# Kernel optimization log

Measured on AMD Instinct MI355X. Metric: run time of the kernel, lower is better.

The kernel has to match this reference:

```python
import jax, jax.numpy as jnp
import numpy as np

B, S, D = 4, 4096, 64

def setup_inputs() -> dict:
    key = jax.random.key(0)
    kq, kk, kv = jax.random.split(key, 3)
    return {
        "q": jax.random.normal(kq, (B, S, D), dtype=jnp.float32),
        "k": jax.random.normal(kk, (B, S, D), dtype=jnp.float32),
        "v": jax.random.normal(kv, (B, S, D), dtype=jnp.float32),
    }

def reference(q, k, v):
    # scores: [B, Sq, Sk]; NOTE: scale is k.shape[-1] (not sqrt), per the source.
    scores = jnp.einsum("bqd,bkd->bqk", q, k) / k.shape[-1]
    # softmax over dim=1 == the QUERY axis (non-standard), then matmul V.
    probs = jax.nn.softmax(scores, axis=1)            # [B, Sq, Sk]
    attn = jnp.einsum("bqk,bkd->bqd", probs, v)       # [B, Sq, D]
    attn_w = jax.nn.softmax(attn, axis=1)             # softmax over Sq again
    return (attn, attn_w)
```

## Files before the change

### kernel.cpp

```cpp
#include <hip/hip_runtime.h>
#include <hip/hip_bf16.h>
#include <math.h>

#define BB 4
#define SS 4096
#define DD 64
#define KSPLIT 4
#define QSPLIT 8

typedef __attribute__((ext_vector_type(8))) short short8;
typedef __attribute__((ext_vector_type(4))) float f32x4;
typedef __attribute__((ext_vector_type(2))) unsigned int u32x2;
typedef unsigned int u32;
typedef unsigned short ushort_t;

#define MFMA16(a,b,c) __builtin_amdgcn_mfma_f32_16x16x32_bf16((a),(b),(c),0,0,0)
#define C2SC 0.022542110700140054f

union Pk8 { short8 s8; u32 u[4]; u32x2 h[2]; };

static __device__ __forceinline__ unsigned short f2bf(float f) {
  union { float f; u32 u; } x; x.f = f;
  u32 r = (x.u + 0x7FFFu + ((x.u >> 16) & 1u)) >> 16;
  return (unsigned short)r;
}

static __device__ __forceinline__ u32 pk2(float a, float b) {
  return (u32)f2bf(a) | ((u32)f2bf(b) << 16);
}

static __device__ __forceinline__ void gload16(const void* g, void* l) {
  __builtin_amdgcn_global_load_lds((const __attribute__((address_space(1))) u32*)g,
                                   (__attribute__((address_space(3))) u32*)l, 16, 0, 0);
}

__global__ __launch_bounds__(256) void p0_convert(
    const float* __restrict__ q, const float* __restrict__ k,
    ushort_t* __restrict__ QB, ushort_t* __restrict__ KB,
    float* __restrict__ out0, float* __restrict__ z2)
{
  const size_t i = (size_t)blockIdx.x * 256 + threadIdx.x;
  float4 a = ((const float4*)q)[i];
  float4 c = ((const float4*)k)[i];
  ((ushort4*)QB)[i] = make_ushort4(f2bf(a.x), f2bf(a.y), f2bf(a.z), f2bf(a.w));
  ((ushort4*)KB)[i] = make_ushort4(f2bf(c.x), f2bf(c.y), f2bf(c.z), f2bf(c.w));
  ((float4*)out0)[i] = make_float4(0.f, 0.f, 0.f, 0.f);
  if (blockIdx.x == 0) z2[threadIdx.x] = 0.f;
}

__global__ __launch_bounds__(256, 4) void pa_colsum(
    const ushort_t* __restrict__ QB, const ushort_t* __restrict__ KB,
    float* __restrict__ Zp)
{
  const int kb0 = blockIdx.x * 128;
  const int qch = blockIdx.y;
  const int b   = blockIdx.z;
  const int t = threadIdx.x, w = t >> 6, lane = t & 63;
  const int g = lane >> 4, r15 = lane & 15;
  const int r8 = lane >> 3, c8 = lane & 7;
  const int QCH = SS / QSPLIT;
  const int NT = QCH / 64;

  __shared__ alignas(16) char qbuf[2][64*128];

  short8 ak[2][2];
#pragma unroll
  for (int s = 0; s < 2; ++s)
#pragma unroll
    for (int dh = 0; dh < 2; ++dh)
      ak[s][dh] = *(const short8*)(KB + ((size_t)b*SS + kb0 + 32*w + 16*s + r15)*DD + 32*dh + 8*g);

  {
    const int q0 = qch * QCH;
#pragma unroll
    for (int j = 0; j < 2; ++j) {
      const int rl = 16*w + 8*j + r8;
      const char* gsrc = (const char*)(QB + ((size_t)b*SS + q0 + rl)*DD) + 16*(c8 ^ r8);
      gload16(gsrc, qbuf[0] + (16*w + 8*j)*128);
    }
  }
  asm volatile("s_waitcnt vmcnt(0)" ::: "memory");
  __syncthreads();

  float z[8];
#pragma unroll
  for (int i = 0; i < 8; ++i) z[i] = 0.f;

  int cur = 0;
  for (int tt = 0; tt < NT; ++tt) {
    if (tt < NT-1) {
      const int q0 = qch*QCH + (tt+1)*64;
#pragma unroll
      for (int j = 0; j < 2; ++j) {
        const int rl = 16*w + 8*j + r8;
        const char* gsrc = (const char*)(QB + ((size_t)b*SS + q0 + rl)*DD) + 16*(c8 ^ r8);
        gload16(gsrc, qbuf[cur^1] + (16*w + 8*j)*128);
      }
    }
    const char* qb = qbuf[cur];
#pragma unroll
    for (int qt = 0; qt < 4; ++qt) {
      const int qrow = 16*qt + r15;
      const char* base = qb + qrow*128;
      short8 bq0 = *(const short8*)(base + 16*((g    ) ^ (qrow & 7)));
      short8 bq1 = *(const short8*)(base + 16*((4 + g) ^ (qrow & 7)));
#pragma unroll
      for (int s = 0; s < 2; ++s) {
        f32x4 acc = {0.f,0.f,0.f,0.f};
        acc = MFMA16(ak[s][0], bq0, acc);
        acc = MFMA16(ak[s][1], bq1, acc);
        z[4*s+0] += exp2f(acc[0]*C2SC); z[4*s+1] += exp2f(acc[1]*C2SC);
        z[4*s+2] += exp2f(acc[2]*C2SC); z[4*s+3] += exp2f(acc[3]*C2SC);
      }
    }
    asm volatile("s_waitcnt vmcnt(0)" ::: "memory");
    __syncthreads();
    cur ^= 1;
  }
#pragma unroll
  for (int m = 1; m < 16; m <<= 1)
#pragma unroll
    for (int i = 0; i < 8; ++i) z[i] += __shfl_xor(z[i], m);
  if (r15 == 0) {
#pragma unroll
    for (int s = 0; s < 2; ++s)
#pragma unroll
      for (int r = 0; r < 4; ++r)
        Zp[((size_t)qch*BB + b)*SS + kb0 + 32*w + 16*s + 4*g + r] = z[4*s+r];
  }
}

__global__ __launch_bounds__(256) void p2_vt(
    const float* __restrict__ v, const float* __restrict__ Zp,
    ushort_t* __restrict__ VT)
{
  const int k0 = blockIdx.x * 64;
  const int b  = blockIdx.y;
  const int t = threadIdx.x;
  __shared__ float vs[64][65];
  __shared__ float izs[64];
  {
    const int row = t >> 2, cq = (t & 3) * 16;
    const float* src = v + ((size_t)b*SS + k0 + row)*DD + cq;
#pragma unroll
    for (int i = 0; i < 4; ++i) {
      float4 x = ((const float4*)src)[i];
      vs[row][cq + 4*i + 0] = x.x; vs[row][cq + 4*i + 1] = x.y;
      vs[row][cq + 4*i + 2] = x.z; vs[row][cq + 4*i + 3] = x.w;
    }
  }
  if (t < 64) {
    float z = 0.f;
#pragma unroll
    for (int c = 0; c < QSPLIT; ++c)
      z += Zp[((size_t)c*BB + b)*SS + k0 + t];
    izs[t] = 1.0f / z;
  }
  __syncthreads();
  const int d = t >> 2, ks = (t & 3) * 16;
  u32* dst = (u32*)VT + (((size_t)b*DD + d)*SS + k0 + ks)/2;
#pragma unroll
  for (int i = 0; i < 8; ++i) {
    float a0 = vs[ks + 2*i    ][d] * izs[ks + 2*i    ];
    float a1 = vs[ks + 2*i + 1][d] * izs[ks + 2*i + 1];
    dst[i] = (u32)f2bf(a0) | ((u32)f2bf(a1) << 16);
  }
}

__global__ __launch_bounds__(256, 3) void pb_attn(
    const ushort_t* __restrict__ QB, const ushort_t* __restrict__ KB,
    const ushort_t* __restrict__ VT, float* __restrict__ out0)
{
  const int q0 = blockIdx.x * 64;
  const int kbase = blockIdx.y * (SS / KSPLIT);
  const int b  = blockIdx.z;
  const int t = threadIdx.x, w = t >> 6, lane = t & 63;
  const int g = lane >> 4, r15 = lane & 15;
  const int NT = SS / KSPLIT / 128;

  __shared__ alignas(16) char kbuf[128*128];
  __shared__ alignas(16) char vbuf[64*256];

  short8 aq[4][2];
#pragma unroll
  for (int qt = 0; qt < 4; ++qt)
#pragma unroll
    for (int dh = 0; dh < 2; ++dh)
      aq[qt][dh] = *(const short8*)(QB + ((size_t)b*SS + q0 + 16*qt + r15)*DD + 32*dh + 8*g);

  f32x4 acc[4][4];
#pragma unroll
  for (int qt = 0; qt < 4; ++qt)
#pragma unroll
    for (int dt = 0; dt < 4; ++dt) acc[qt][dt] = (f32x4){0.f,0.f,0.f,0.f};

  for (int kt = 0; kt < NT; ++kt) {
    const int k0 = kbase + kt*128;
#pragma unroll
    for (int j = 0; j < 4; ++j) {
      const int row = 32*j + 8*w + (lane >> 3);
      const char* gsrc = (const char*)(KB + ((size_t)b*SS + k0 + row)*DD) + 16*((lane & 7) ^ (row & 7));
      gload16(gsrc, kbuf + (32*j + 8*w)*128);
    }
#pragma unroll
    for (int j = 0; j < 4; ++j) {
      const int row = 16*j + 4*w + (lane >> 4);
      const char* gsrc = (const char*)(VT + ((size_t)b*DD + row)*SS + k0) + 16*((lane & 15) ^ (row & 15));
      gload16(gsrc, vbuf + (16*j + 4*w)*256);
    }
    asm volatile("s_waitcnt vmcnt(0)" ::: "memory");
    __syncthreads();

    u32 pk[2][4][2];
#pragma unroll
    for (int s = 0; s < 2; ++s) {
      const int rowA = 64*s + 16*w + r15;
      const char* base = kbuf + rowA*128;
      short8 ka0 = *(const short8*)(base + 16*((g    ) ^ (rowA & 7)));
      short8 ka1 = *(const short8*)(base + 16*((4 + g) ^ (rowA & 7)));
#pragma unroll
      for (int qt = 0; qt < 4; ++qt) {
        f32x4 a = {0.f,0.f,0.f,0.f};
        a = MFMA16(ka0, aq[qt][0], a);
        a = MFMA16(ka1, aq[qt][1], a);
        pk[s][qt][0] = pk2(exp2f(a[0]*C2SC), exp2f(a[1]*C2SC));
        pk[s][qt][1] = pk2(exp2f(a[2]*C2SC), exp2f(a[3]*C2SC));
      }
    }
    Pk8 ap[4];
#pragma unroll
    for (int qt = 0; qt < 4; ++qt) {
      ap[qt].u[0] = pk[0][qt][0]; ap[qt].u[1] = pk[0][qt][1];
      ap[qt].u[2] = pk[1][qt][0]; ap[qt].u[3] = pk[1][qt][1];
    }
    const int cA = 2*w + (g >> 1);
    const int cB = 8 + 2*w + (g >> 1);
    const int sub8 = 8*(g & 1);
#pragma unroll
    for (int dt = 0; dt < 4; ++dt) {
      const int vrow = 16*dt + r15;
      Pk8 bv;
      bv.h[0] = *(const u32x2*)(vbuf + vrow*256 + 16*(cA ^ r15) + sub8);
      bv.h[1] = *(const u32x2*)(vbuf + vrow*256 + 16*(cB ^ r15) + sub8);
#pragma unroll
      for (int qt = 0; qt < 4; ++qt)
        acc[qt][dt] = MFMA16(ap[qt].s8, bv.s8, acc[qt][dt]);
    }
    __syncthreads();
  }

  f32x4* r0 = (f32x4*)kbuf;
  f32x4* r1 = (f32x4*)vbuf;
  if (w == 1) {
#pragma unroll
    for (int qt = 0; qt < 4; ++qt)
#pragma unroll
      for (int dt = 0; dt < 4; ++dt) r0[(qt*4+dt)*64 + lane] = acc[qt][dt];
  }
  if (w == 2) {
#pragma unroll
    for (int qt = 0; qt < 4; ++qt)
#pragma unroll
      for (int dt = 0; dt < 4; ++dt) r1[(qt*4+dt)*64 + lane] = acc[qt][dt];
  }
  __syncthreads();
  if (w == 0) {
#pragma unroll
    for (int qt = 0; qt < 4; ++qt)
#pragma unroll
      for (int dt = 0; dt < 4; ++dt)
        acc[qt][dt] += r0[(qt*4+dt)*64 + lane] + r1[(qt*4+dt)*64 + lane];
  }
  __syncthreads();
  if (w == 3) {
#pragma unroll
    for (int qt = 0; qt < 4; ++qt)
#pragma unroll
      for (int dt = 0; dt < 4; ++dt) r0[(qt*4+dt)*64 + lane] = acc[qt][dt];
  }
  __syncthreads();
  if (w == 0) {
#pragma unroll
    for (int qt = 0; qt < 4; ++qt)
#pragma unroll
      for (int dt = 0; dt < 4; ++dt) {
        f32x4 s = acc[qt][dt] + r0[(qt*4+dt)*64 + lane];
#pragma unroll
        for (int rr = 0; rr < 4; ++rr)
          atomicAdd(&out0[((size_t)b*SS + q0 + 16*qt + 4*g + rr)*DD + 16*dt + r15], s[rr]);
      }
  }
}

__global__ __launch_bounds__(256) void k4f(
    const float* __restrict__ attn, float* __restrict__ z2)
{
  const int b = blockIdx.x;
  const int q0 = blockIdx.y * 32;
  const int t = threadIdx.x;
  const int d = t & 63, rg = t >> 6;
  float ze = 0.f;
#pragma unroll
  for (int i = 0; i < 8; ++i) {
    float a = attn[((size_t)b*SS + q0 + 4*i + rg)*DD + d];
    ze += __expf(a);
  }
  __shared__ float red[4][64];
  red[rg][d] = ze;
  __syncthreads();
  if (t < 64)
    atomicAdd(&z2[b*DD + t], red[0][t] + red[1][t] + red[2][t] + red[3][t]);
}

__global__ __launch_bounds__(256) void k6w(
    const float* __restrict__ attn, const float* __restrict__ z2,
    float* __restrict__ out1)
{
  const size_t i = (size_t)blockIdx.x * 256 + threadIdx.x;
  const int b = (int)(i >> 18);
  const int d = (int)(i & 63);
  out1[i] = __expf(attn[i]) / z2[b*DD + d];
}

extern "C" void kernel_launch(void* const* d_in, const int* in_sizes, int n_in,
                              void* d_out, int out_size, void* d_ws, size_t ws_size,
                              hipStream_t stream) {
  const float* q = (const float*)d_in[0];
  const float* k = (const float*)d_in[1];
  const float* v = (const float*)d_in[2];
  float* out0 = (float*)d_out;
  float* out1 = out0 + (size_t)BB * SS * DD;

  ushort_t* QB = (ushort_t*)out1;
  ushort_t* KB = QB + (size_t)BB * SS * DD;

  float* ws = (float*)d_ws;
  ushort_t* VT = (ushort_t*)ws;
  float* Zp = (float*)(VT + (size_t)BB * DD * SS);
  float* z2 = Zp + (size_t)QSPLIT * BB * SS;

  hipLaunchKernelGGL(p0_convert, dim3(BB*SS*DD/4/256), dim3(256), 0, stream, q, k, QB, KB, out0, z2);
  hipLaunchKernelGGL(pa_colsum, dim3(SS/128, QSPLIT, BB), dim3(256), 0, stream, QB, KB, Zp);
  hipLaunchKernelGGL(p2_vt, dim3(SS/64, BB), dim3(256), 0, stream, v, Zp, VT);
  hipLaunchKernelGGL(pb_attn, dim3(SS/64, KSPLIT, BB), dim3(256), 0, stream, QB, KB, VT, out0);
  hipLaunchKernelGGL(k4f, dim3(BB, SS/32), dim3(256), 0, stream, out0, z2);
  hipLaunchKernelGGL(k6w, dim3(BB*SS*DD/256), dim3(256), 0, stream, out0, z2, out1);
}
```

Measured before the change: 87.79 us.

## Replace LDS staging with direct register double-buffered global loads in colsum and attn

Both the column-sum and attention kernels stop staging Q/K/V tiles through shared memory with global_load_lds and barriers. Each wave now loads its MFMA operands straight from global memory into registers, alternating between two register buffers so the next tile's loads overlap the current tile's compute. The attention kernel's final cross-wave reduction now uses a single shared array and one barrier, and its occupancy hint drops to 2 blocks per SM to make room for the extra registers. pk2 switches to the library bf16 conversion. The trade-off is more redundant global/L2 traffic and register pressure in exchange for removing LDS round-trips and per-tile barriers.

```diff
diff --git a/kernel.cpp b/kernel.cpp
--- a/kernel.cpp
+++ b/kernel.cpp
@@ -26,12 +26,11 @@
 }
 
 static __device__ __forceinline__ u32 pk2(float a, float b) {
-  return (u32)f2bf(a) | ((u32)f2bf(b) << 16);
-}
-
-static __device__ __forceinline__ void gload16(const void* g, void* l) {
-  __builtin_amdgcn_global_load_lds((const __attribute__((address_space(1))) u32*)g,
-                                   (__attribute__((address_space(3))) u32*)l, 16, 0, 0);
+  __hip_bfloat16 lo = __float2bfloat16(a);
+  __hip_bfloat16 hi = __float2bfloat16(b);
+  unsigned short ls, hs;
+  __builtin_memcpy(&ls, &lo, 2); __builtin_memcpy(&hs, &hi, 2);
+  return (u32)ls | ((u32)hs << 16);
 }
 
 __global__ __launch_bounds__(256) void p0_convert(
@@ -48,6 +47,31 @@
   if (blockIdx.x == 0) z2[threadIdx.x] = 0.f;
 }
 
+static __device__ __forceinline__ void load_q4(
+    short8 bq[4][2], const ushort_t* __restrict__ QB, size_t qrow, int g)
+{
+#pragma unroll
+  for (int qt = 0; qt < 4; ++qt)
+#pragma unroll
+    for (int dh = 0; dh < 2; ++dh)
+      bq[qt][dh] = *(const short8*)(QB + (qrow + 16*qt)*DD + 32*dh + 8*g);
+}
+
+static __device__ __forceinline__ void pa_tile(
+    const short8 ak[2][2], const short8 bq[4][2], float z[8])
+{
+#pragma unroll
+  for (int qt = 0; qt < 4; ++qt)
+#pragma unroll
+    for (int s = 0; s < 2; ++s) {
+      f32x4 a = {0.f,0.f,0.f,0.f};
+      a = MFMA16(ak[s][0], bq[qt][0], a);
+      a = MFMA16(ak[s][1], bq[qt][1], a);
+      z[4*s+0] += exp2f(a[0]*C2SC); z[4*s+1] += exp2f(a[1]*C2SC);
+      z[4*s+2] += exp2f(a[2]*C2SC); z[4*s+3] += exp2f(a[3]*C2SC);
+    }
+}
+
 __global__ __launch_bounds__(256, 4) void pa_colsum(
     const ushort_t* __restrict__ QB, const ushort_t* __restrict__ KB,
     float* __restrict__ Zp)
@@ -57,11 +81,7 @@
   const int b   = blockIdx.z;
   const int t = threadIdx.x, w = t >> 6, lane = t & 63;
   const int g = lane >> 4, r15 = lane & 15;
-  const int r8 = lane >> 3, c8 = lane & 7;
   const int QCH = SS / QSPLIT;
-  const int NT = QCH / 64;
-
-  __shared__ alignas(16) char qbuf[2][64*128];
 
   short8 ak[2][2];
 #pragma unroll
@@ -70,53 +90,22 @@
     for (int dh = 0; dh < 2; ++dh)
       ak[s][dh] = *(const short8*)(KB + ((size_t)b*SS + kb0 + 32*w + 16*s + r15)*DD + 32*dh + 8*g);
 
-  {
-    const int q0 = qch * QCH;
-#pragma unroll
-    for (int j = 0; j < 2; ++j) {
-      const int rl = 16*w + 8*j + r8;
-      const char* gsrc = (const char*)(QB + ((size_t)b*SS + q0 + rl)*DD) + 16*(c8 ^ r8);
-      gload16(gsrc, qbuf[0] + (16*w + 8*j)*128);
-    }
-  }
-  asm volatile("s_waitcnt vmcnt(0)" ::: "memory");
-  __syncthreads();
-
   float z[8];
 #pragma unroll
   for (int i = 0; i < 8; ++i) z[i] = 0.f;
 
-  int cur = 0;
-  for (int tt = 0; tt < NT; ++tt) {
-    if (tt < NT-1) {
-      const int q0 = qch*QCH + (tt+1)*64;
-#pragma unroll
-      for (int j = 0; j < 2; ++j) {
-        const int rl = 16*w + 8*j + r8;
-        const char* gsrc = (const char*)(QB + ((size_t)b*SS + q0 + rl)*DD) + 16*(c8 ^ r8);
-        gload16(gsrc, qbuf[cur^1] + (16*w + 8*j)*128);
-      }
-    }
-    const char* qb = qbuf[cur];
-#pragma unroll
-    for (int qt = 0; qt < 4; ++qt) {
-      const int qrow = 16*qt + r15;
-      const char* base = qb + qrow*128;
-      short8 bq0 = *(const short8*)(base + 16*((g    ) ^ (qrow & 7)));
-      short8 bq1 = *(const short8*)(base + 16*((4 + g) ^ (qrow & 7)));
-#pragma unroll
-      for (int s = 0; s < 2; ++s) {
-        f32x4 acc = {0.f,0.f,0.f,0.f};
-        acc = MFMA16(ak[s][0], bq0, acc);
-        acc = MFMA16(ak[s][1], bq1, acc);
-        z[4*s+0] += exp2f(acc[0]*C2SC); z[4*s+1] += exp2f(acc[1]*C2SC);
-        z[4*s+2] += exp2f(acc[2]*C2SC); z[4*s+3] += exp2f(acc[3]*C2SC);
-      }
-    }
-    asm volatile("s_waitcnt vmcnt(0)" ::: "memory");
-    __syncthreads();
-    cur ^= 1;
-  }
+  const size_t qrow0 = (size_t)b*SS + qch*QCH + r15;
+  short8 bqA[4][2], bqB[4][2];
+  load_q4(bqA, QB, qrow0, g);
+
+#pragma unroll 1
+  for (int tt = 0; tt < QCH/64; tt += 2) {
+    load_q4(bqB, QB, qrow0 + (size_t)(tt+1)*64, g);
+    pa_tile(ak, bqA, z);
+    if (tt + 2 < QCH/64) load_q4(bqA, QB, qrow0 + (size_t)(tt+2)*64, g);
+    pa_tile(ak, bqB, z);
+  }
+
 #pragma unroll
   for (int m = 1; m < 16; m <<= 1)
 #pragma unroll
@@ -167,7 +156,55 @@
   }
 }
 
-__global__ __launch_bounds__(256, 3) void pb_attn(
+static __device__ __forceinline__ void load_k2(
+    short8 ka[2][2], const ushort_t* __restrict__ KB, size_t krow, int g)
+{
+#pragma unroll
+  for (int s = 0; s < 2; ++s)
+#pragma unroll
+    for (int dh = 0; dh < 2; ++dh)
+      ka[s][dh] = *(const short8*)(KB + (krow + 64*s)*DD + 32*dh + 8*g);
+}
+
+static __device__ __forceinline__ void load_v4(
+    short8 bv[4], const ushort_t* __restrict__ VT, size_t voff)
+{
+#pragma unroll
+  for (int dt = 0; dt < 4; ++dt) {
+    Pk8 u;
+    u.h[0] = *(const u32x2*)(VT + voff + (size_t)16*dt*SS);
+    u.h[1] = *(const u32x2*)(VT + voff + (size_t)16*dt*SS + 64);
+    bv[dt] = u.s8;
+  }
+}
+
+static __device__ __forceinline__ void pb_tile(
+    const short8 ka[2][2], const short8 bv[4], const short8 aq[4][2],
+    f32x4 acc[4][4])
+{
+  u32 pk[2][4][2];
+#pragma unroll
+  for (int s = 0; s < 2; ++s)
+#pragma unroll
+    for (int qt = 0; qt < 4; ++qt) {
+      f32x4 a = {0.f,0.f,0.f,0.f};
+      a = MFMA16(ka[s][0], aq[qt][0], a);
+      a = MFMA16(ka[s][1], aq[qt][1], a);
+      pk[s][qt][0] = pk2(exp2f(a[0]*C2SC), exp2f(a[1]*C2SC));
+      pk[s][qt][1] = pk2(exp2f(a[2]*C2SC), exp2f(a[3]*C2SC));
+    }
+#pragma unroll
+  for (int qt = 0; qt < 4; ++qt) {
+    Pk8 ap;
+    ap.u[0] = pk[0][qt][0]; ap.u[1] = pk[0][qt][1];
+    ap.u[2] = pk[1][qt][0]; ap.u[3] = pk[1][qt][1];
+#pragma unroll
+    for (int dt = 0; dt < 4; ++dt)
+      acc[qt][dt] = MFMA16(ap.s8, bv[dt], acc[qt][dt]);
+  }
+}
+
+__global__ __launch_bounds__(256, 2) void pb_attn(
     const ushort_t* __restrict__ QB, const ushort_t* __restrict__ KB,
     const ushort_t* __restrict__ VT, float* __restrict__ out0)
 {
@@ -178,8 +215,7 @@
   const int g = lane >> 4, r15 = lane & 15;
   const int NT = SS / KSPLIT / 128;
 
-  __shared__ alignas(16) char kbuf[128*128];
-  __shared__ alignas(16) char vbuf[64*256];
+  __shared__ f32x4 red[3][16][64];
 
   short8 aq[4][2];
 #pragma unroll
@@ -194,97 +230,39 @@
 #pragma unroll
     for (int dt = 0; dt < 4; ++dt) acc[qt][dt] = (f32x4){0.f,0.f,0.f,0.f};
 
-  for (int kt = 0; kt < NT; ++kt) {
-    const int k0 = kbase + kt*128;
-#pragma unroll
-    for (int j = 0; j < 4; ++j) {
-      const int row = 32*j + 8*w + (lane >> 3);
-      const char* gsrc = (const char*)(KB + ((size_t)b*SS + k0 + row)*DD) + 16*((lane & 7) ^ (row & 7));
-      gload16(gsrc, kbuf + (32*j + 8*w)*128);
+  const size_t krow0 = (size_t)b*SS + kbase + 16*w + r15;
+  const size_t voff0 = ((size_t)b*DD + r15)*SS + kbase + 16*w + 4*g;
+
+  short8 kaA[2][2], kaB[2][2], bvA[4], bvB[4];
+  load_k2(kaA, KB, krow0, g);
+  load_v4(bvA, VT, voff0);
+
+#pragma unroll 1
+  for (int kt = 0; kt < NT; kt += 2) {
+    load_k2(kaB, KB, krow0 + (size_t)(kt+1)*128, g);
+    load_v4(bvB, VT, voff0 + (size_t)(kt+1)*128);
+    pb_tile(kaA, bvA, aq, acc);
+    if (kt + 2 < NT) {
+      load_k2(kaA, KB, krow0 + (size_t)(kt+2)*128, g);
+      load_v4(bvA, VT, voff0 + (size_t)(kt+2)*128);
     }
-#pragma unroll
-    for (int j = 0; j < 4; ++j) {
-      const int row = 16*j + 4*w + (lane >> 4);
-      const char* gsrc = (const char*)(VT + ((size_t)b*DD + row)*SS + k0) + 16*((lane & 15) ^ (row & 15));
-      gload16(gsrc, vbuf + (16*j + 4*w)*256);
-    }
-    asm volatile("s_waitcnt vmcnt(0)" ::: "memory");
-    __syncthreads();
-
-    u32 pk[2][4][2];
-#pragma unroll
-    for (int s = 0; s < 2; ++s) {
-      const int rowA = 64*s + 16*w + r15;
-      const char* base = kbuf + rowA*128;
-      short8 ka0 = *(const short8*)(base + 16*((g    ) ^ (rowA & 7)));
-      short8 ka1 = *(const short8*)(base + 16*((4 + g) ^ (rowA & 7)));
-#pragma unroll
-      for (int qt = 0; qt < 4; ++qt) {
-        f32x4 a = {0.f,0.f,0.f,0.f};
-        a = MFMA16(ka0, aq[qt][0], a);
-        a = MFMA16(ka1, aq[qt][1], a);
-        pk[s][qt][0] = pk2(exp2f(a[0]*C2SC), exp2f(a[1]*C2SC));
-        pk[s][qt][1] = pk2(exp2f(a[2]*C2SC), exp2f(a[3]*C2SC));
-      }
-    }
-    Pk8 ap[4];
-#pragma unroll
-    for (int qt = 0; qt < 4; ++qt) {
-      ap[qt].u[0] = pk[0][qt][0]; ap[qt].u[1] = pk[0][qt][1];
-      ap[qt].u[2] = pk[1][qt][0]; ap[qt].u[3] = pk[1][qt][1];
-    }
-    const int cA = 2*w + (g >> 1);
-    const int cB = 8 + 2*w + (g >> 1);
-    const int sub8 = 8*(g & 1);
-#pragma unroll
-    for (int dt = 0; dt < 4; ++dt) {
-      const int vrow = 16*dt + r15;
-      Pk8 bv;
-      bv.h[0] = *(const u32x2*)(vbuf + vrow*256 + 16*(cA ^ r15) + sub8);
-      bv.h[1] = *(const u32x2*)(vbuf + vrow*256 + 16*(cB ^ r15) + sub8);
-#pragma unroll
-      for (int qt = 0; qt < 4; ++qt)
-        acc[qt][dt] = MFMA16(ap[qt].s8, bv.s8, acc[qt][dt]);
-    }
-    __syncthreads();
-  }
-
-  f32x4* r0 = (f32x4*)kbuf;
-  f32x4* r1 = (f32x4*)vbuf;
-  if (w == 1) {
+    pb_tile(kaB, bvB, aq, acc);
+  }
+
+  if (w > 0) {
 #pragma unroll
     for (int qt = 0; qt < 4; ++qt)
 #pragma unroll
-      for (int dt = 0; dt < 4; ++dt) r0[(qt*4+dt)*64 + lane] = acc[qt][dt];
-  }
-  if (w == 2) {
-#pragma unroll
-    for (int qt = 0; qt < 4; ++qt)
-#pragma unroll
-      for (int dt = 0; dt < 4; ++dt) r1[(qt*4+dt)*64 + lane] = acc[qt][dt];
+      for (int dt = 0; dt < 4; ++dt) red[w-1][qt*4+dt][lane] = acc[qt][dt];
   }
   __syncthreads();
   if (w == 0) {
 #pragma unroll
     for (int qt = 0; qt < 4; ++qt)
 #pragma unroll
-      for (int dt = 0; dt < 4; ++dt)
-        acc[qt][dt] += r0[(qt*4+dt)*64 + lane] + r1[(qt*4+dt)*64 + lane];
-  }
-  __syncthreads();
-  if (w == 3) {
-#pragma unroll
-    for (int qt = 0; qt < 4; ++qt)
-#pragma unroll
-      for (int dt = 0; dt < 4; ++dt) r0[(qt*4+dt)*64 + lane] = acc[qt][dt];
-  }
-  __syncthreads();
-  if (w == 0) {
-#pragma unroll
-    for (int qt = 0; qt < 4; ++qt)
-#pragma unroll
       for (int dt = 0; dt < 4; ++dt) {
-        f32x4 s = acc[qt][dt] + r0[(qt*4+dt)*64 + lane];
+        f32x4 s = acc[qt][dt] + red[0][qt*4+dt][lane]
+                + red[1][qt*4+dt][lane] + red[2][qt*4+dt][lane];
 #pragma unroll
         for (int rr = 0; rr < 4; ++rr)
           atomicAdd(&out0[((size_t)b*SS + q0 + 16*qt + 4*g + rr)*DD + 16*dt + r15], s[rr]);
```

Result: slower. 111.5 us (+27.0%).
